# Optimization experiments

Measured on AMD Instinct MI355X. Metric: run time of the kernel, lower is better.

## Reference

```python
import jax, jax.numpy as jnp
import numpy as np

EPS = 1e-6

def _rmsnorm(x, w):
    var = jnp.mean(x * x, axis=-1, keepdims=True)
    return x * jax.lax.rsqrt(var + EPS) * w

def _act_quant(x):
    # per-token int8 absmax quantization (BitNet b1.58)
    scale = 127.0 / jnp.clip(jnp.max(jnp.abs(x), axis=-1, keepdims=True), 1e-5)
    return jnp.round(jnp.clip(x * scale, -128.0, 127.0)) / scale

def _weight_quant(w):
    # per-tensor ternary quantization with mean-abs scale
    scale = 1.0 / jnp.clip(jnp.mean(jnp.abs(w)), 1e-5)
    return jnp.round(jnp.clip(w * scale, -1.0, 1.0)) / scale

def _ste(x, qfn):
    return x + jax.lax.stop_gradient(qfn(x) - x)

def _bitlinear(x, w):
    xq = _ste(x, _act_quant)
    wq = _ste(w, _weight_quant)
    return jnp.einsum('bsh,fh->bsf', xq, wq)

def setup_inputs() -> dict:
    key = jax.random.key(0)
    k1, k2, k3 = jax.random.split(key, 3)
    B, S, H, F = 4, 4096, 1024, 4096
    x = jax.random.normal(k1, (B, S, H), dtype=jnp.float32)
    norm_w = jnp.ones((H,), dtype=jnp.float32)
    w_up = jax.random.normal(k2, (F, H), dtype=jnp.float32) * (H ** -0.5)
    w_down = jax.random.normal(k3, (H, F), dtype=jnp.float32) * (F ** -0.5)
    return {"x": x, "norm_w": norm_w, "w_up": w_up, "w_down": w_down}

def reference(x, norm_w, w_up, w_down):
    residual = x
    h = _rmsnorm(x, norm_w)
    h = _bitlinear(h, w_up)          # [B,S,F]
    h = jnp.square(jax.nn.relu(h))   # relu^2
    h = _bitlinear(h, w_down)        # [B,S,H]
    return h + residual
```

## Files before the change

kernel.cpp:

```cpp
#include <hip/hip_runtime.h>
#include <hip/hip_fp16.h>

#define M_TOK 16384
#define H_DIM 1024
#define F_DIM 4096

typedef __attribute__((ext_vector_type(4))) int int4v;

static const size_t OFF_H2    = 0;
static const size_t OFF_Q2    = OFF_H2   + 134217728ULL;
static const size_t OFF_XQ    = OFF_Q2   + 67108864ULL;
static const size_t OFF_WQU   = OFF_XQ   + 16777216ULL;
static const size_t OFF_WQD   = OFF_WQU  + 4194304ULL;
static const size_t OFF_DQX   = OFF_WQD  + 4194304ULL;
static const size_t OFF_DQ2   = OFF_DQX  + 65536ULL;
static const size_t OFF_PMAX  = OFF_DQ2  + 65536ULL;
static const size_t OFF_WPART = OFF_PMAX + 4194304ULL;
static const size_t OFF_WSC   = OFF_WPART+ 8192ULL;
static const size_t WS_NEEDED = OFF_WSC  + 16ULL;

__device__ __forceinline__ void ldg_lds16(const void* g, void* l) {
  __builtin_amdgcn_global_load_lds(
      (const __attribute__((address_space(1))) void*)g,
      (__attribute__((address_space(3))) void*)l, 16, 0, 0);
}

__global__ __launch_bounds__(256) void k_wabs(const float* __restrict__ wu,
                                              const float* __restrict__ wd,
                                              float* __restrict__ part) {
  const int b = blockIdx.x;
  const float* w = (b < 1024) ? wu : wd;
  const int cb = b & 1023;
  const size_t base = (size_t)cb * 4096 + threadIdx.x * 4;
  float s = 0.0f;
#pragma unroll
  for (int it = 0; it < 4; ++it) {
    const float4 v = *(const float4*)(w + base + it * 1024);
    s += fabsf(v.x) + fabsf(v.y) + fabsf(v.z) + fabsf(v.w);
  }
#pragma unroll
  for (int sh = 32; sh; sh >>= 1) s += __shfl_xor(s, sh, 64);
  __shared__ float red[4];
  if ((threadIdx.x & 63) == 0) red[threadIdx.x >> 6] = s;
  __syncthreads();
  if (threadIdx.x == 0) part[b] = red[0] + red[1] + red[2] + red[3];
}

__global__ __launch_bounds__(256) void k_wscale(const float* __restrict__ part,
                                                float* __restrict__ wsc) {
  const int b = blockIdx.x;
  const float* p = part + b * 1024;
  float s = p[threadIdx.x] + p[threadIdx.x + 256] + p[threadIdx.x + 512] + p[threadIdx.x + 768];
#pragma unroll
  for (int sh = 32; sh; sh >>= 1) s += __shfl_xor(s, sh, 64);
  __shared__ float red[4];
  if ((threadIdx.x & 63) == 0) red[threadIdx.x >> 6] = s;
  __syncthreads();
  if (threadIdx.x == 0) {
    const float mean = (red[0] + red[1] + red[2] + red[3]) * (1.0f / 4194304.0f);
    const float c = fmaxf(mean, 1e-5f);
    wsc[b * 2]     = c;
    wsc[b * 2 + 1] = 1.0f / c;
  }
}

__global__ __launch_bounds__(256) void k_wquant(const float* __restrict__ wu,
                                                const float* __restrict__ wd,
                                                char* __restrict__ qu,
                                                char* __restrict__ qd,
                                                const float* __restrict__ wsc) {
  const size_t t = (size_t)blockIdx.x * 256 + threadIdx.x;
  const float* w; char* q; float scale; size_t i;
  if (t < 1048576) { w = wu; q = qu; scale = wsc[1]; i = t * 4; }
  else             { w = wd; q = qd; scale = wsc[3]; i = (t - 1048576) * 4; }
  const float4 v = *(const float4*)(w + i);
  const int a = (int)rintf(fminf(fmaxf(v.x * scale, -1.0f), 1.0f));
  const int b = (int)rintf(fminf(fmaxf(v.y * scale, -1.0f), 1.0f));
  const int c = (int)rintf(fminf(fmaxf(v.z * scale, -1.0f), 1.0f));
  const int d = (int)rintf(fminf(fmaxf(v.w * scale, -1.0f), 1.0f));
  *(unsigned*)(q + i) = (a & 255) | ((b & 255) << 8) | ((c & 255) << 16) | ((d & 255) << 24);
}

__global__ __launch_bounds__(256) void k_rmsnorm_quant(const float* __restrict__ x,
                                                       const float* __restrict__ nw,
                                                       char* __restrict__ xq,
                                                       float* __restrict__ dqx) {
  const int row = blockIdx.x;
  const int t = threadIdx.x;
  const float4 v = *(const float4*)(x + (size_t)row * H_DIM + t * 4);
  float ss = v.x * v.x + v.y * v.y + v.z * v.z + v.w * v.w;
#pragma unroll
  for (int sh = 32; sh; sh >>= 1) ss += __shfl_xor(ss, sh, 64);
  __shared__ float red[4];
  __shared__ float redm[4];
  if ((t & 63) == 0) red[t >> 6] = ss;
  __syncthreads();
  ss = red[0] + red[1] + red[2] + red[3];
  const float rinv = 1.0f / sqrtf(ss * (1.0f / 1024.0f) + 1e-6f);
  const float4 w4 = *(const float4*)(nw + t * 4);
  float4 n;
  n.x = v.x * rinv * w4.x;  n.y = v.y * rinv * w4.y;
  n.z = v.z * rinv * w4.z;  n.w = v.w * rinv * w4.w;
  float am = fmaxf(fmaxf(fabsf(n.x), fabsf(n.y)), fmaxf(fabsf(n.z), fabsf(n.w)));
#pragma unroll
  for (int sh = 32; sh; sh >>= 1) am = fmaxf(am, __shfl_xor(am, sh, 64));
  if ((t & 63) == 0) redm[t >> 6] = am;
  __syncthreads();
  am = fmaxf(fmaxf(redm[0], redm[1]), fmaxf(redm[2], redm[3]));
  am = fmaxf(am, 1e-5f);
  const float scale = 127.0f / am;
  const int qa = (int)rintf(fminf(fmaxf(n.x * scale, -128.0f), 127.0f));
  const int qb = (int)rintf(fminf(fmaxf(n.y * scale, -128.0f), 127.0f));
  const int qc = (int)rintf(fminf(fmaxf(n.z * scale, -128.0f), 127.0f));
  const int qd = (int)rintf(fminf(fmaxf(n.w * scale, -128.0f), 127.0f));
  *(unsigned*)(xq + (size_t)row * H_DIM + t * 4) =
      (qa & 255) | ((qb & 255) << 8) | ((qc & 255) << 16) | ((qd & 255) << 24);
  if (t == 0) dqx[row] = am * (1.0f / 127.0f);
}

#define MFMA_I8(i, j, av, bv) \
  acc[i][j] = __builtin_amdgcn_mfma_i32_16x16x64_i8(av, bv, acc[i][j], 0, 0, 0)

#define MFMA16(IB) \
  __builtin_amdgcn_s_setprio(1); \
  MFMA_I8(IB + 0, 0, a0, b0); MFMA_I8(IB + 0, 1, a0, b1); MFMA_I8(IB + 0, 2, a0, b2); MFMA_I8(IB + 0, 3, a0, b3); \
  MFMA_I8(IB + 1, 0, a1, b0); MFMA_I8(IB + 1, 1, a1, b1); MFMA_I8(IB + 1, 2, a1, b2); MFMA_I8(IB + 1, 3, a1, b3); \
  MFMA_I8(IB + 2, 0, a2, b0); MFMA_I8(IB + 2, 1, a2, b1); MFMA_I8(IB + 2, 2, a2, b2); MFMA_I8(IB + 2, 3, a2, b3); \
  MFMA_I8(IB + 3, 0, a3, b0); MFMA_I8(IB + 3, 1, a3, b1); MFMA_I8(IB + 3, 2, a3, b2); MFMA_I8(IB + 3, 3, a3, b3); \
  __builtin_amdgcn_s_setprio(0)

template <int LDA_, int LDB_, int KT>
__device__ __forceinline__ void gemm_core4p(const char* __restrict__ A,
                                            const char* __restrict__ B,
                                            int mBase, int nBase,
                                            char* __restrict__ smem,
                                            int4v acc[8][4]) {
  const int t = threadIdx.x;
  const int lane = t & 63;
  const int w = t >> 6;
  const int wm = w & 1;
  const int wn = w >> 1;
  const int sRow = t >> 3;
  const int sSeg = (t & 7) ^ (sRow & 7);
  const char* Ag = A + (size_t)(mBase + sRow) * LDA_ + sSeg * 16;
  const char* Bg = B + (size_t)(nBase + sRow) * LDB_ + sSeg * 16;
  const int q  = lane >> 4;
  const int fr = lane & 15;
  const int sw = fr & 7;
  const int s0 = ((q) ^ sw) << 4;
  const int s1 = ((4 + q) ^ sw) << 4;
  const int rA = wm * 128 + fr;
  const int rB = wn * 64 + fr;
  const int dst = t << 4;

#define STG_A(Q, KTI, BUFO) \
  ldg_lds16(Ag + (size_t)((Q) * 64) * LDA_ + (size_t)(KTI) * 128, \
            smem + (BUFO) + (Q) * 8192 + dst)
#define STG_B(Q, KTI, BUFO) \
  ldg_lds16(Bg + (size_t)((Q) * 64) * LDB_ + (size_t)(KTI) * 128, \
            smem + (BUFO) + 32768 + (Q) * 8192 + dst)

  STG_B(0, 0, 0); STG_B(1, 0, 0); STG_B(2, 0, 0); STG_B(3, 0, 0);
  STG_A(0, 0, 0); STG_A(2, 0, 0); STG_A(1, 0, 0); STG_A(3, 0, 0);
  asm volatile("s_waitcnt vmcnt(2)\n\ts_barrier" ::: "memory");

  int cur = 0;
  for (int kt = 0; kt < KT; ++kt) {
    const int nxt = cur ^ 65536;
    const char* Ab = smem + cur;
    const char* Bb = smem + cur + 32768;
    int4v a0, a1, a2, a3, b0, b1, b2, b3;
    a0 = *(const int4v*)(Ab + (rA +  0) * 128 + s0);
    a1 = *(const int4v*)(Ab + (rA + 16) * 128 + s0);
    a2 = *(const int4v*)(Ab + (rA + 32) * 128 + s0);
    a3 = *(const int4v*)(Ab + (rA + 48) * 128 + s0);
    b0 = *(const int4v*)(Bb + (rB +  0) * 128 + s0);
    b1 = *(const int4v*)(Bb + (rB + 16) * 128 + s0);
    b2 = *(const int4v*)(Bb + (rB + 32) * 128 + s0);
    b3 = *(const int4v*)(Bb + (rB + 48) * 128 + s0);
    if (kt + 1 < KT) { STG_B(0, kt + 1, nxt); STG_B(1, kt + 1, nxt); }
    MFMA16(0);
    if (kt + 1 < KT) { asm volatile("s_waitcnt vmcnt(2)\n\ts_barrier" ::: "memory"); }
    else             { asm volatile("s_waitcnt vmcnt(0)\n\ts_barrier" ::: "memory"); }
    a0 = *(const int4v*)(Ab + (rA +  64) * 128 + s0);
    a1 = *(const int4v*)(Ab + (rA +  80) * 128 + s0);
    a2 = *(const int4v*)(Ab + (rA +  96) * 128 + s0);
    a3 = *(const int4v*)(Ab + (rA + 112) * 128 + s0);
    if (kt + 1 < KT) { STG_B(2, kt + 1, nxt); STG_B(3, kt + 1, nxt); }
    MFMA16(4);
    a0 = *(const int4v*)(Ab + (rA +  0) * 128 + s1);
    a1 = *(const int4v*)(Ab + (rA + 16) * 128 + s1);
    a2 = *(const int4v*)(Ab + (rA + 32) * 128 + s1);
    a3 = *(const int4v*)(Ab + (rA + 48) * 128 + s1);
    b0 = *(const int4v*)(Bb + (rB +  0) * 128 + s1);
    b1 = *(const int4v*)(Bb + (rB + 16) * 128 + s1);
    b2 = *(const int4v*)(Bb + (rB + 32) * 128 + s1);
    b3 = *(const int4v*)(Bb + (rB + 48) * 128 + s1);
    if (kt + 1 < KT) { STG_A(0, kt + 1, nxt); STG_A(2, kt + 1, nxt); }
    MFMA16(0);
    a0 = *(const int4v*)(Ab + (rA +  64) * 128 + s1);
    a1 = *(const int4v*)(Ab + (rA +  80) * 128 + s1);
    a2 = *(const int4v*)(Ab + (rA +  96) * 128 + s1);
    a3 = *(const int4v*)(Ab + (rA + 112) * 128 + s1);
    if (kt + 1 < KT) { STG_A(1, kt + 1, nxt); STG_A(3, kt + 1, nxt); }
    MFMA16(4);
    asm volatile("s_waitcnt vmcnt(2)\n\ts_barrier" ::: "memory");
    cur = nxt;
  }
#undef STG_A
#undef STG_B
}

__global__ __launch_bounds__(512, 2) void k_gemm1(const char* __restrict__ xq,
                                                  const char* __restrict__ wq,
                                                  const float* __restrict__ wsc,
                                                  const float* __restrict__ dqx,
                                                  __half* __restrict__ h2,
                                                  float* __restrict__ pmax) {
  __shared__ char smem[131072];
  int4v acc[8][4];
#pragma unroll
  for (int i = 0; i < 8; ++i)
#pragma unroll
    for (int j = 0; j < 4; ++j) acc[i][j] = (int4v){0, 0, 0, 0};
  const int mBase = blockIdx.x * 256;
  const int nBase = blockIdx.y * 256;
  gemm_core4p<H_DIM, H_DIM, 8>(xq, wq, mBase, nBase, smem, acc);

  const int t = threadIdx.x;
  const int lane = t & 63;
  const int w = t >> 6;
  const int wm = w & 1;
  const int wn = w >> 1;
  const int q  = lane >> 4;
  const int fr = lane & 15;
  const float dqw = wsc[0];
#pragma unroll
  for (int i = 0; i < 8; ++i) {
    const int rbase = mBase + wm * 128 + i * 16 + (q << 2);
    const float4 dq4 = *(const float4*)(dqx + rbase);
    const float* dqp = (const float*)&dq4;
    float rmax[4] = {0.0f, 0.0f, 0.0f, 0.0f};
#pragma unroll
    for (int j = 0; j < 4; ++j) {
      const int col = nBase + wn * 64 + j * 16 + fr;
#pragma unroll
      for (int r = 0; r < 4; ++r) {
        float v = (float)acc[i][j][r] * dqp[r] * dqw;
        v = fmaxf(v, 0.0f);
        v = v * v;
        const __half h = __float2half(v);
        h2[(size_t)(rbase + r) * F_DIM + col] = h;
        rmax[r] = fmaxf(rmax[r], __half2float(h));
      }
    }
#pragma unroll
    for (int s = 1; s < 16; s <<= 1) {
#pragma unroll
      for (int r = 0; r < 4; ++r) rmax[r] = fmaxf(rmax[r], __shfl_xor(rmax[r], s, 64));
    }
    if (fr == 0) {
      const int nb2 = blockIdx.y * 4 + wn;
#pragma unroll
      for (int r = 0; r < 4; ++r) pmax[(size_t)nb2 * M_TOK + rbase + r] = rmax[r];
    }
  }
}

__global__ __launch_bounds__(256) void k_quant2(const __half* __restrict__ h2,
                                                const float* __restrict__ pmax,
                                                char* __restrict__ q2,
                                                float* __restrict__ dq2) {
  const int row = blockIdx.x;
  const int t = threadIdx.x;
  __shared__ float sm;
  if (t < 64) {
    float m = pmax[(size_t)t * M_TOK + row];
#pragma unroll
    for (int sh = 32; sh; sh >>= 1) m = fmaxf(m, __shfl_xor(m, sh, 64));
    if (t == 0) sm = fmaxf(m, 1e-5f);
  }
  __syncthreads();
  const float mx = sm;
  const float s = 127.0f / mx;
  if (t == 0) dq2[row] = mx * (1.0f / 127.0f);
  const size_t i = (size_t)row * F_DIM + t * 16;
  __half2 hh[8];
  *(float4*)(hh)     = *(const float4*)(h2 + i);
  *(float4*)(hh + 4) = *(const float4*)(h2 + i + 8);
  unsigned u[4];
#pragma unroll
  for (int k = 0; k < 4; ++k) {
    const int q0 = (int)rintf(fminf(__low2float(hh[2 * k]) * s, 127.0f));
    const int q1 = (int)rintf(fminf(__high2float(hh[2 * k]) * s, 127.0f));
    const int q2i = (int)rintf(fminf(__low2float(hh[2 * k + 1]) * s, 127.0f));
    const int q3 = (int)rintf(fminf(__high2float(hh[2 * k + 1]) * s, 127.0f));
    u[k] = (q0 & 255) | ((q1 & 255) << 8) | ((q2i & 255) << 16) | ((q3 & 255) << 24);
  }
  *(uint4*)(q2 + i) = make_uint4(u[0], u[1], u[2], u[3]);
}

__global__ __launch_bounds__(512, 2) void k_gemm2(const char* __restrict__ q2,
                                                  const char* __restrict__ wq,
                                                  const float* __restrict__ wsc,
                                                  const float* __restrict__ dq2,
                                                  const float* __restrict__ x,
                                                  float* __restrict__ out) {
  __shared__ char smem[131072];
  int4v acc[8][4];
#pragma unroll
  for (int i = 0; i < 8; ++i)
#pragma unroll
    for (int j = 0; j < 4; ++j) acc[i][j] = (int4v){0, 0, 0, 0};
  const int mBase = blockIdx.x * 256;
  const int nBase = blockIdx.y * 256;
  gemm_core4p<F_DIM, F_DIM, 32>(q2, wq, mBase, nBase, smem, acc);

  const int t = threadIdx.x;
  const int lane = t & 63;
  const int w = t >> 6;
  const int wm = w & 1;
  const int wn = w >> 1;
  const int q  = lane >> 4;
  const int fr = lane & 15;
  const float dqw = wsc[2];
#pragma unroll
  for (int i = 0; i < 8; ++i) {
    const int rbase = mBase + wm * 128 + i * 16 + (q << 2);
    const float4 dq4 = *(const float4*)(dq2 + rbase);
    const float* dqp = (const float*)&dq4;
#pragma unroll
    for (int j = 0; j < 4; ++j) {
      const int col = nBase + wn * 64 + j * 16 + fr;
#pragma unroll
      for (int r = 0; r < 4; ++r) {
        const size_t idx = (size_t)(rbase + r) * H_DIM + col;
        out[idx] = (float)acc[i][j][r] * dqp[r] * dqw + x[idx];
      }
    }
  }
}

extern "C" void kernel_launch(void* const* d_in, const int* in_sizes, int n_in,
                              void* d_out, int out_size, void* d_ws, size_t ws_size,
                              hipStream_t stream) {
  const float* x  = (const float*)d_in[0];
  const float* nw = (const float*)d_in[1];
  const float* wu = (const float*)d_in[2];
  const float* wd = (const float*)d_in[3];
  float* out = (float*)d_out;
  char* ws = (char*)d_ws;
  if (ws_size < WS_NEEDED) return;

  __half* h2     = (__half*)(ws + OFF_H2);
  char* q2       = ws + OFF_Q2;
  char* xq       = ws + OFF_XQ;
  char* wqu      = ws + OFF_WQU;
  char* wqd      = ws + OFF_WQD;
  float* dqx     = (float*)(ws + OFF_DQX);
  float* dq2     = (float*)(ws + OFF_DQ2);
  float* pmax    = (float*)(ws + OFF_PMAX);
  float* wpart   = (float*)(ws + OFF_WPART);
  float* wsc     = (float*)(ws + OFF_WSC);

  k_wabs<<<2048, 256, 0, stream>>>(wu, wd, wpart);
  k_wscale<<<2, 256, 0, stream>>>(wpart, wsc);
  k_wquant<<<8192, 256, 0, stream>>>(wu, wd, wqu, wqd, wsc);
  k_rmsnorm_quant<<<M_TOK, 256, 0, stream>>>(x, nw, xq, dqx);
  k_gemm1<<<dim3(M_TOK / 256, F_DIM / 256), 512, 0, stream>>>(xq, wqu, wsc, dqx, h2, pmax);
  k_quant2<<<M_TOK, 256, 0, stream>>>(h2, pmax, q2, dq2);
  k_gemm2<<<dim3(M_TOK / 256, H_DIM / 256), 512, 0, stream>>>(q2, wqd, wsc, dq2, x, out);
}
```

Baseline: 333.8 us.

## Fuse second activation quantization into down-projection GEMM A-tile loading

Replaces the standalone quant2 kernel with a tiny row-scale kernel, and has gemm2 load fp16 activations directly and quantize them to int8 in registers before writing to LDS. This removes writing and re-reading the int8 intermediate buffer. In exchange, each fp16 row is read once per output-column block, doubling bytes per read relative to int8. It also adds conversion work and manual vmcnt-based pipelining inside the GEMM main loop.

```diff
diff --git a/kernel.cpp b/kernel.cpp
--- a/kernel.cpp
+++ b/kernel.cpp
@@ -6,10 +6,11 @@
 #define F_DIM 4096
 
 typedef __attribute__((ext_vector_type(4))) int int4v;
+typedef __attribute__((ext_vector_type(4))) float f32x4;
 
 static const size_t OFF_H2    = 0;
-static const size_t OFF_Q2    = OFF_H2   + 134217728ULL;
-static const size_t OFF_XQ    = OFF_Q2   + 67108864ULL;
+static const size_t OFF_RS2   = OFF_H2   + 134217728ULL;
+static const size_t OFF_XQ    = OFF_RS2  + 67108864ULL;
 static const size_t OFF_WQU   = OFF_XQ   + 16777216ULL;
 static const size_t OFF_WQD   = OFF_WQU  + 4194304ULL;
 static const size_t OFF_DQX   = OFF_WQD  + 4194304ULL;
@@ -23,6 +24,12 @@
   __builtin_amdgcn_global_load_lds(
       (const __attribute__((address_space(1))) void*)g,
       (__attribute__((address_space(3))) void*)l, 16, 0, 0);
+}
+
+__device__ __forceinline__ void gload32(const void* p, f32x4& a, f32x4& b) {
+  asm volatile("global_load_dwordx4 %0, %2, off\n\t"
+               "global_load_dwordx4 %1, %2, off offset:16"
+               : "=&v"(a), "=&v"(b) : "v"(p) : "memory");
 }
 
 __global__ __launch_bounds__(256) void k_wabs(const float* __restrict__ wu,
@@ -267,43 +274,159 @@
   }
 }
 
-__global__ __launch_bounds__(256) void k_quant2(const __half* __restrict__ h2,
-                                                const float* __restrict__ pmax,
-                                                char* __restrict__ q2,
-                                                float* __restrict__ dq2) {
-  const int row = blockIdx.x;
+__global__ __launch_bounds__(256) void k_rowscale(const float* __restrict__ pmax,
+                                                  float* __restrict__ dq2,
+                                                  float* __restrict__ rs2) {
+  const int row = blockIdx.x * 256 + threadIdx.x;
+  float m = 0.0f;
+#pragma unroll
+  for (int p = 0; p < 64; ++p) m = fmaxf(m, pmax[(size_t)p * M_TOK + row]);
+  m = fmaxf(m, 1e-5f);
+  dq2[row] = m * (1.0f / 127.0f);
+  rs2[row] = 127.0f / m;
+}
+
+__device__ __forceinline__ void cvt_write_q(const f32x4& va, const f32x4& vb,
+                                            float s, char* d) {
+  union { f32x4 f[2]; __half2 h[8]; } u;
+  u.f[0] = va; u.f[1] = vb;
+  unsigned o[4];
+#pragma unroll
+  for (int p = 0; p < 4; ++p) {
+    const float f0 = __low2float(u.h[2 * p]);
+    const float f1 = __high2float(u.h[2 * p]);
+    const float f2 = __low2float(u.h[2 * p + 1]);
+    const float f3 = __high2float(u.h[2 * p + 1]);
+    const int q0 = (int)rintf(fminf(f0 * s, 127.0f));
+    const int q1 = (int)rintf(fminf(f1 * s, 127.0f));
+    const int q2 = (int)rintf(fminf(f2 * s, 127.0f));
+    const int q3 = (int)rintf(fminf(f3 * s, 127.0f));
+    o[p] = (q0 & 255) | ((q1 & 255) << 8) | ((q2 & 255) << 16) | ((q3 & 255) << 24);
+  }
+  *(uint4*)d = make_uint4(o[0], o[1], o[2], o[3]);
+}
+
+template <int KT>
+__device__ __forceinline__ void gemm2_core(const __half* __restrict__ H,
+                                           const char* __restrict__ B,
+                                           const float* __restrict__ rs2,
+                                           int mBase, int nBase,
+                                           char* __restrict__ smem,
+                                           int4v acc[8][4]) {
   const int t = threadIdx.x;
-  __shared__ float sm;
-  if (t < 64) {
-    float m = pmax[(size_t)t * M_TOK + row];
-#pragma unroll
-    for (int sh = 32; sh; sh >>= 1) m = fmaxf(m, __shfl_xor(m, sh, 64));
-    if (t == 0) sm = fmaxf(m, 1e-5f);
-  }
-  __syncthreads();
-  const float mx = sm;
-  const float s = 127.0f / mx;
-  if (t == 0) dq2[row] = mx * (1.0f / 127.0f);
-  const size_t i = (size_t)row * F_DIM + t * 16;
-  __half2 hh[8];
-  *(float4*)(hh)     = *(const float4*)(h2 + i);
-  *(float4*)(hh + 4) = *(const float4*)(h2 + i + 8);
-  unsigned u[4];
-#pragma unroll
-  for (int k = 0; k < 4; ++k) {
-    const int q0 = (int)rintf(fminf(__low2float(hh[2 * k]) * s, 127.0f));
-    const int q1 = (int)rintf(fminf(__high2float(hh[2 * k]) * s, 127.0f));
-    const int q2i = (int)rintf(fminf(__low2float(hh[2 * k + 1]) * s, 127.0f));
-    const int q3 = (int)rintf(fminf(__high2float(hh[2 * k + 1]) * s, 127.0f));
-    u[k] = (q0 & 255) | ((q1 & 255) << 8) | ((q2i & 255) << 16) | ((q3 & 255) << 24);
-  }
-  *(uint4*)(q2 + i) = make_uint4(u[0], u[1], u[2], u[3]);
-}
-
-__global__ __launch_bounds__(512, 2) void k_gemm2(const char* __restrict__ q2,
+  const int lane = t & 63;
+  const int w = t >> 6;
+  const int wm = w & 1;
+  const int wn = w >> 1;
+  const int sRow = t >> 3;
+  const int sSeg = (t & 7) ^ (sRow & 7);
+  const __half* Hg = H + (size_t)(mBase + sRow) * F_DIM + sSeg * 16;
+  const char*   Bg = B + (size_t)(nBase + sRow) * F_DIM + sSeg * 16;
+  const int q  = lane >> 4;
+  const int fr = lane & 15;
+  const int sw = fr & 7;
+  const int s0 = ((q) ^ sw) << 4;
+  const int s1 = ((4 + q) ^ sw) << 4;
+  const int rA = wm * 128 + fr;
+  const int rB = wn * 64 + fr;
+  const int dst = t << 4;
+
+  float rs[4];
+#pragma unroll
+  for (int Q = 0; Q < 4; ++Q) rs[Q] = rs2[mBase + Q * 64 + sRow];
+  asm volatile("s_waitcnt vmcnt(0)" ::: "memory");
+  __builtin_amdgcn_sched_barrier(0);
+
+#define STG_B2(Q, KTI, BUFO) \
+  ldg_lds16(Bg + (size_t)((Q) * 64) * F_DIM + (size_t)(KTI) * 128, \
+            smem + (BUFO) + 32768 + (Q) * 8192 + dst)
+#define GLD_A(arr, i0, Q, KTI) \
+  gload32(Hg + (size_t)(Q) * 64 * F_DIM + (size_t)(KTI) * 128, arr[i0], arr[i0 + 1])
+
+  f32x4 a01[4];
+  f32x4 a23[4];
+
+  GLD_A(a01, 0, 0, 0); GLD_A(a01, 2, 1, 0);
+  GLD_A(a23, 0, 2, 0); GLD_A(a23, 2, 3, 0);
+  STG_B2(0, 0, 0); STG_B2(1, 0, 0); STG_B2(2, 0, 0); STG_B2(3, 0, 0);
+  asm volatile("s_waitcnt vmcnt(4)" ::: "memory");
+  __builtin_amdgcn_sched_barrier(0);
+  cvt_write_q(a01[0], a01[1], rs[0], smem + 0 * 8192 + dst);
+  cvt_write_q(a01[2], a01[3], rs[1], smem + 1 * 8192 + dst);
+  cvt_write_q(a23[0], a23[1], rs[2], smem + 2 * 8192 + dst);
+  cvt_write_q(a23[2], a23[3], rs[3], smem + 3 * 8192 + dst);
+  GLD_A(a01, 0, 0, 1); GLD_A(a01, 2, 1, 1);
+  asm volatile("s_waitcnt lgkmcnt(0)" ::: "memory");
+  asm volatile("s_waitcnt vmcnt(4)\n\ts_barrier" ::: "memory");
+
+  int cur = 0;
+  for (int kt = 0; kt < KT; ++kt) {
+    const int nxt = cur ^ 65536;
+    const char* Ab = smem + cur;
+    const char* Bb = smem + cur + 32768;
+    int4v a0, a1, a2, a3, b0, b1, b2, b3;
+    a0 = *(const int4v*)(Ab + (rA +  0) * 128 + s0);
+    a1 = *(const int4v*)(Ab + (rA + 16) * 128 + s0);
+    a2 = *(const int4v*)(Ab + (rA + 32) * 128 + s0);
+    a3 = *(const int4v*)(Ab + (rA + 48) * 128 + s0);
+    b0 = *(const int4v*)(Bb + (rB +  0) * 128 + s0);
+    b1 = *(const int4v*)(Bb + (rB + 16) * 128 + s0);
+    b2 = *(const int4v*)(Bb + (rB + 32) * 128 + s0);
+    b3 = *(const int4v*)(Bb + (rB + 48) * 128 + s0);
+    if (kt + 1 < KT) {
+      STG_B2(0, kt + 1, nxt); STG_B2(1, kt + 1, nxt);
+      GLD_A(a23, 0, 2, kt + 1); GLD_A(a23, 2, 3, kt + 1);
+    }
+    MFMA16(0);
+    a0 = *(const int4v*)(Ab + (rA +  64) * 128 + s0);
+    a1 = *(const int4v*)(Ab + (rA +  80) * 128 + s0);
+    a2 = *(const int4v*)(Ab + (rA +  96) * 128 + s0);
+    a3 = *(const int4v*)(Ab + (rA + 112) * 128 + s0);
+    if (kt + 1 < KT) { STG_B2(2, kt + 1, nxt); STG_B2(3, kt + 1, nxt); }
+    MFMA16(4);
+    a0 = *(const int4v*)(Ab + (rA +  0) * 128 + s1);
+    a1 = *(const int4v*)(Ab + (rA + 16) * 128 + s1);
+    a2 = *(const int4v*)(Ab + (rA + 32) * 128 + s1);
+    a3 = *(const int4v*)(Ab + (rA + 48) * 128 + s1);
+    b0 = *(const int4v*)(Bb + (rB +  0) * 128 + s1);
+    b1 = *(const int4v*)(Bb + (rB + 16) * 128 + s1);
+    b2 = *(const int4v*)(Bb + (rB + 32) * 128 + s1);
+    b3 = *(const int4v*)(Bb + (rB + 48) * 128 + s1);
+    if (kt + 1 < KT) {
+      asm volatile("s_waitcnt vmcnt(8)" ::: "memory");
+      __builtin_amdgcn_sched_barrier(0);
+      cvt_write_q(a01[0], a01[1], rs[0], smem + nxt + 0 * 8192 + dst);
+      cvt_write_q(a01[2], a01[3], rs[1], smem + nxt + 1 * 8192 + dst);
+    }
+    MFMA16(0);
+    a0 = *(const int4v*)(Ab + (rA +  64) * 128 + s1);
+    a1 = *(const int4v*)(Ab + (rA +  80) * 128 + s1);
+    a2 = *(const int4v*)(Ab + (rA +  96) * 128 + s1);
+    a3 = *(const int4v*)(Ab + (rA + 112) * 128 + s1);
+    if (kt + 1 < KT) {
+      asm volatile("s_waitcnt vmcnt(2)" ::: "memory");
+      __builtin_amdgcn_sched_barrier(0);
+      cvt_write_q(a23[0], a23[1], rs[2], smem + nxt + 2 * 8192 + dst);
+      cvt_write_q(a23[2], a23[3], rs[3], smem + nxt + 3 * 8192 + dst);
+    }
+    if (kt + 2 < KT) { GLD_A(a01, 0, 0, kt + 2); GLD_A(a01, 2, 1, kt + 2); }
+    MFMA16(4);
+    if (kt + 1 < KT) {
+      asm volatile("s_waitcnt lgkmcnt(0)" ::: "memory");
+      if (kt + 2 < KT) { asm volatile("s_waitcnt vmcnt(4)\n\ts_barrier" ::: "memory"); }
+      else             { asm volatile("s_waitcnt vmcnt(0)\n\ts_barrier" ::: "memory"); }
+    }
+    cur = nxt;
+  }
+#undef STG_B2
+#undef GLD_A
+}
+
+__global__ __launch_bounds__(512, 2) void k_gemm2(const __half* __restrict__ h2,
                                                   const char* __restrict__ wq,
                                                   const float* __restrict__ wsc,
                                                   const float* __restrict__ dq2,
+                                                  const float* __restrict__ rs2,
                                                   const float* __restrict__ x,
                                                   float* __restrict__ out) {
   __shared__ char smem[131072];
@@ -314,7 +437,7 @@
     for (int j = 0; j < 4; ++j) acc[i][j] = (int4v){0, 0, 0, 0};
   const int mBase = blockIdx.x * 256;
   const int nBase = blockIdx.y * 256;
-  gemm_core4p<F_DIM, F_DIM, 32>(q2, wq, mBase, nBase, smem, acc);
+  gemm2_core<32>(h2, wq, rs2, mBase, nBase, smem, acc);
 
   const int t = threadIdx.x;
   const int lane = t & 63;
@@ -353,7 +476,7 @@
   if (ws_size < WS_NEEDED) return;
 
   __half* h2     = (__half*)(ws + OFF_H2);
-  char* q2       = ws + OFF_Q2;
+  float* rs2     = (float*)(ws + OFF_RS2);
   char* xq       = ws + OFF_XQ;
   char* wqu      = ws + OFF_WQU;
   char* wqd      = ws + OFF_WQD;
@@ -368,6 +491,6 @@
   k_wquant<<<8192, 256, 0, stream>>>(wu, wd, wqu, wqd, wsc);
   k_rmsnorm_quant<<<M_TOK, 256, 0, stream>>>(x, nw, xq, dqx);
   k_gemm1<<<dim3(M_TOK / 256, F_DIM / 256), 512, 0, stream>>>(xq, wqu, wsc, dqx, h2, pmax);
-  k_quant2<<<M_TOK, 256, 0, stream>>>(h2, pmax, q2, dq2);
-  k_gemm2<<<dim3(M_TOK / 256, H_DIM / 256), 512, 0, stream>>>(q2, wqd, wsc, dq2, x, out);
-}
+  k_rowscale<<<M_TOK / 256, 256, 0, stream>>>(pmax, dq2, rs2);
+  k_gemm2<<<dim3(M_TOK / 256, H_DIM / 256), 512, 0, stream>>>(h2, wqd, wsc, dq2, rs2, x, out);
+}
```

After: 334.0 us. Within noise of the previous version (+0.1%).
